# Kernel optimization log

Hardware: AMD Instinct MI355X
Metric: run time of the kernel (lower is better)

Reference implementation:

```python
import jax, jax.numpy as jnp
import numpy as np

ALPHA = 0.2  # LeakyReLU slope in GAT
OUT_SLOPE = 0.01  # default nn.LeakyyReLU slope for self.out
B, E, IN_DIM, HID, HEADS = 4, 2048, 32, 18, 3
DH = HID // HEADS  # per-head out dim = 6


def _leaky(x, slope):
    return jnp.where(x > 0, x, slope * x)


def _gat_head(x, adj, W, a):
    # x: [B,E,in], W: [in,dh], a: [2*dh,1]
    h = jnp.einsum('bei,id->bed', x, W)                      # [B,E,dh]
    d = h.shape[-1]
    # score[b,i,j] = leakyrelu(a . concat(h_i, h_j)) = leakyrelu(h_i.a1 + h_j.a2)
    e1 = jnp.einsum('bed,d->be', h, a[:d, 0])
    e2 = jnp.einsum('bed,d->be', h, a[d:, 0])
    score = _leaky(e1[:, :, None] + e2[:, None, :], ALPHA)   # [B,E,E]
    scores = jnp.where(adj == 1.0, score, 0.0)
    logits = jnp.where(adj > 0.0, scores, -30.0)
    att = jax.nn.softmax(logits, axis=2)                     # softmax over j
    # h_prime[b,j,d] = sum_i att[b,i,j] * h[b,i,d]  (torch sums over dim=1)
    h_prime = jnp.einsum('bij,bid->bjd', att, h)
    return jax.nn.elu(h_prime)  # concat=True -> elu


def _gat_multihead(x, adj, Ws, As):
    # Ws: [H,in,dh], As: [H,2*dh,1]
    outs = jax.vmap(lambda W, a: _gat_head(x, adj, W, a))(Ws, As)  # [H,B,E,dh]
    H, b, e, d = outs.shape
    return jnp.moveaxis(outs, 0, 2).reshape(b, e, H * d)  # concat heads last-dim


def _gcn(x, adj2d, W, b):
    return adj2d @ (x @ W) + b


def setup_inputs() -> dict:
    key = jax.random.key(0)
    ks = jax.random.split(key, 16)
    node_input = jax.random.normal(ks[0], (B, E, IN_DIM), jnp.float32)
    uv_filed = jax.random.normal(ks[1], (B, E, IN_DIM), jnp.float32)
    adj = jax.random.randint(ks[2], (B, E, E), 0, 2).astype(jnp.float32)
    s = 0.1
    Wt1 = jax.random.normal(ks[3], (HEADS, IN_DIM, DH), jnp.float32) * s
    at1 = jax.random.normal(ks[4], (HEADS, 2 * DH, 1), jnp.float32) * s
    Wt2 = jax.random.normal(ks[5], (HEADS, IN_DIM, DH), jnp.float32) * s
    at2 = jax.random.normal(ks[6], (HEADS, 2 * DH, 1), jnp.float32) * s
    Wg1 = jax.random.normal(ks[7], (HID, 16), jnp.float32) * s
    bg1 = jnp.zeros((16,), jnp.float32)
    Wg2 = jax.random.normal(ks[8], (16, 2), jnp.float32) * s
    bg2 = jnp.zeros((2,), jnp.float32)
    Wo1 = jax.random.normal(ks[9], (HID, 16), jnp.float32) * s
    bo1 = jnp.zeros((16,), jnp.float32)
    Wo2 = jax.random.normal(ks[10], (16, 2), jnp.float32) * s
    bo2 = jnp.zeros((2,), jnp.float32)
    return dict(node_input=node_input, uv_filed=uv_filed, adj=adj,
                Wt1=Wt1, at1=at1, Wt2=Wt2, at2=at2,
                Wg1=Wg1, bg1=bg1, Wg2=Wg2, bg2=bg2,
                Wo1=Wo1, bo1=bo1, Wo2=Wo2, bo2=bo2)


def reference(node_input, uv_filed, adj, Wt1, at1, Wt2, at2,
              Wg1, bg1, Wg2, bg2, Wo1, bo1, Wo2, bo2):
    h = _gat_multihead(node_input, adj, Wt1, at1)  # [B,E,18]
    o = _gat_multihead(uv_filed, adj, Wt2, at2)    # [B,E,18]
    a0 = adj[0]
    Y = jax.nn.relu(_gcn(h[0], a0, Wg1, bg1))
    O = jax.nn.relu(_gcn(o[0], a0, Wo1, bo1))
    Y = _gcn(Y, a0, Wg2, bg2)
    O = _gcn(O, a0, Wo2, bo2)
    return (jax.nn.log_softmax(Y, axis=1), _leaky(O, OUT_SLOPE))
```

## Files before the change

kernel.cpp:

```cpp
#include <hip/hip_runtime.h>
#include <hip/hip_bf16.h>


__global__ __launch_bounds__(256) void kA(
    const float* __restrict__ adj0, unsigned int* __restrict__ bm,
    unsigned int* __restrict__ bmT,
    const float* __restrict__ node, const float* __restrict__ uv,
    const float* __restrict__ Wt1, const float* __restrict__ at1,
    const float* __restrict__ Wt2, const float* __restrict__ at2,
    float* __restrict__ hcol, float* __restrict__ pack1, float* __restrict__ pack2) {
  int b = blockIdx.x;
  if (b < 256) {
    int lane = threadIdx.x & 63, w = threadIdx.x >> 6;
    int t = b * 4 + w;
    int ti = t >> 5, tj = t & 31;
    int row = ti * 64 + lane;
    const float4* ar4 = (const float4*)(adj0 + (size_t)row * 2048 + tj * 64);
    unsigned int rowLo = 0, rowHi = 0, myLo = 0, myHi = 0;
#pragma unroll
    for (int it = 0; it < 16; ++it) {
      float4 v = ar4[it];
      unsigned long long m0 = __ballot(v.x == 1.0f);
      unsigned long long m1 = __ballot(v.y == 1.0f);
      unsigned long long m2 = __ballot(v.z == 1.0f);
      unsigned long long m3 = __ballot(v.w == 1.0f);
      int jb = it * 4;
      if (jb + 0 == lane) { myLo = (unsigned int)m0; myHi = (unsigned int)(m0 >> 32); }
      if (jb + 1 == lane) { myLo = (unsigned int)m1; myHi = (unsigned int)(m1 >> 32); }
      if (jb + 2 == lane) { myLo = (unsigned int)m2; myHi = (unsigned int)(m2 >> 32); }
      if (jb + 3 == lane) { myLo = (unsigned int)m3; myHi = (unsigned int)(m3 >> 32); }
      unsigned int rb = (v.x == 1.0f ? 1u : 0u) | (v.y == 1.0f ? 2u : 0u) |
                        (v.z == 1.0f ? 4u : 0u) | (v.w == 1.0f ? 8u : 0u);
      if (it < 8) rowLo |= rb << (it * 4);
      else rowHi |= rb << ((it - 8) * 4);
    }
    *(uint2*)&bm[(size_t)row * 64 + tj * 2] = make_uint2(rowLo, rowHi);
    int j = tj * 64 + lane;
    *(uint2*)&bmT[(size_t)j * 64 + ti * 2] = make_uint2(myLo, myHi);
    return;
  }
  __shared__ float sW[192];
  __shared__ float sA[12];
  int fb = b - 256;
  int g = fb / 24;
  int h = (fb / 8) % 3;
  int e = (fb % 8) * 256 + threadIdx.x;
  const float* W = (g ? Wt2 : Wt1) + h * 192;
  const float* A = (g ? at2 : at1) + h * 12;
  const float* x = (g ? uv : node) + e * 32;
  if (threadIdx.x < 192) sW[threadIdx.x] = W[threadIdx.x];
  if (threadIdx.x < 12) sA[threadIdx.x] = A[threadIdx.x];
  __syncthreads();
  float xv[32];
#pragma unroll
  for (int i = 0; i < 32; ++i) xv[i] = x[i];
  float hv[6];
#pragma unroll
  for (int d = 0; d < 6; ++d) hv[d] = 0.f;
#pragma unroll
  for (int i = 0; i < 32; ++i)
#pragma unroll
    for (int d = 0; d < 6; ++d) hv[d] += xv[i] * sW[i * 6 + d];
  float e1 = 0.f, e2 = 0.f;
#pragma unroll
  for (int d = 0; d < 6; ++d) {
    e1 += hv[d] * sA[d];
    e2 += hv[d] * sA[6 + d];
  }
  int c = g * 3 + h;
#pragma unroll
  for (int d = 0; d < 6; ++d) hcol[(c * 6 + d) * 2048 + e] = hv[d];
  pack1[c * 2048 + e] = e1;
  pack1[(6 + c) * 2048 + e] = __expf(e1);
  pack1[(12 + c) * 2048 + e] = __expf(0.2f * e1);
  pack2[c * 2048 + e] = e2;
  pack2[(6 + c) * 2048 + e] = __expf(e2);
  pack2[(12 + c) * 2048 + e] = __expf(0.2f * e2);
}

__global__ __launch_bounds__(384) void kB(
    const unsigned int* __restrict__ bm, const float* __restrict__ pack1,
    const float* __restrict__ pack2, const float* __restrict__ hcol,
    float* __restrict__ hsS) {
  int tid = threadIdx.x;
  int c = tid >> 6, lane = tid & 63;
  int i0 = blockIdx.x * 8;
  const float4* p2_4 = (const float4*)pack2;
  float e1r[8], p1r[8], q1r[8], sum[8];
#pragma unroll
  for (int r = 0; r < 8; ++r) {
    e1r[r] = pack1[c * 2048 + i0 + r];
    p1r[r] = pack1[(6 + c) * 2048 + i0 + r];
    q1r[r] = pack1[(12 + c) * 2048 + i0 + r];
    sum[r] = 0.f;
  }
  int sh = (lane & 7) * 4;
#pragma unroll
  for (int it = 0; it < 8; ++it) {
    int j4 = it * 64 + lane;
    float4 e2 = p2_4[c * 512 + j4];
    float4 p2 = p2_4[(6 + c) * 512 + j4];
    float4 q2 = p2_4[(12 + c) * 512 + j4];
    int wbase = it * 8 + (lane >> 3);
    float abx, aby, abz, abw;
#pragma unroll
    for (int r = 0; r < 8; ++r) {
      unsigned int wd = bm[(i0 + r) * 64 + wbase] >> sh;
      { float e = e1r[r] + e2.x; bool p = e > 0.f;
        abx = (p ? p1r[r] : q1r[r]) * (p ? p2.x : q2.x); }
      { float e = e1r[r] + e2.y; bool p = e > 0.f;
        aby = (p ? p1r[r] : q1r[r]) * (p ? p2.y : q2.y); }
      { float e = e1r[r] + e2.z; bool p = e > 0.f;
        abz = (p ? p1r[r] : q1r[r]) * (p ? p2.z : q2.z); }
      { float e = e1r[r] + e2.w; bool p = e > 0.f;
        abw = (p ? p1r[r] : q1r[r]) * (p ? p2.w : q2.w); }
      float s = ((wd & 1u) ? abx : 0.f) + ((wd & 2u) ? aby : 0.f) +
                ((wd & 4u) ? abz : 0.f) + ((wd & 8u) ? abw : 0.f);
      sum[r] += s;
    }
  }
#pragma unroll
  for (int r = 0; r < 8; ++r) {
#pragma unroll
    for (int off = 32; off > 0; off >>= 1) sum[r] += __shfl_xor(sum[r], off);
  }
  if (lane < 6) {
    int row = c * 6 + lane;
#pragma unroll
    for (int r = 0; r < 8; ++r) {
      float inv = 1.0f / sum[r];
      hsS[row * 2048 + i0 + r] = hcol[row * 2048 + i0 + r] * inv;
    }
  }
}

__global__ __launch_bounds__(384) void kC(
    const unsigned int* __restrict__ bmT, const float* __restrict__ pack1,
    const float* __restrict__ pack2, const float* __restrict__ hsS,
    const float* __restrict__ Wg1, const float* __restrict__ Wo1,
    float* __restrict__ T) {
  __shared__ float sW[576];
  __shared__ float sHP[4 * 37];
  int tid = threadIdx.x;
  int c = tid >> 6, L = tid & 63;
  int j0 = blockIdx.x * 4;
  if (tid < 288) { sW[tid] = Wg1[tid]; sW[288 + tid] = Wo1[tid]; }
  int wj[4];
#pragma unroll
  for (int jj = 0; jj < 4; ++jj) wj[jj] = (int)bmT[(size_t)(j0 + jj) * 64 + L];
  float e2v[4], p2v[4], q2v[4];
#pragma unroll
  for (int jj = 0; jj < 4; ++jj) {
    e2v[jj] = pack2[c * 2048 + j0 + jj];
    p2v[jj] = pack2[(6 + c) * 2048 + j0 + jj];
    q2v[jj] = pack2[(12 + c) * 2048 + j0 + jj];
  }
  float acc[4][6];
#pragma unroll
  for (int jj = 0; jj < 4; ++jj)
#pragma unroll
    for (int d = 0; d < 6; ++d) acc[jj][d] = 0.f;

  for (int s = 0; s < 32; ++s) {
    int i = s * 64 + L;
    float e1 = pack1[c * 2048 + i];
    float p1 = pack1[(6 + c) * 2048 + i];
    float q1 = pack1[(12 + c) * 2048 + i];
    float h0 = hsS[(c * 6 + 0) * 2048 + i];
    float h1 = hsS[(c * 6 + 1) * 2048 + i];
    float h2 = hsS[(c * 6 + 2) * 2048 + i];
    float h3 = hsS[(c * 6 + 3) * 2048 + i];
    float h4 = hsS[(c * 6 + 4) * 2048 + i];
    float h5 = hsS[(c * 6 + 5) * 2048 + i];
#pragma unroll
    for (int jj = 0; jj < 4; ++jj) {
      int lo = __builtin_amdgcn_readlane(wj[jj], 2 * s);
      int hi = __builtin_amdgcn_readlane(wj[jj], 2 * s + 1);
      unsigned int wsel = (unsigned int)((L & 32) ? hi : lo);
      float e = e1 + e2v[jj];
      bool pos = e > 0.f;
      float ab = (pos ? p1 : q1) * (pos ? p2v[jj] : q2v[jj]);
      float wgt = ((wsel >> (L & 31)) & 1u) ? ab : 0.f;
      acc[jj][0] += wgt * h0; acc[jj][1] += wgt * h1; acc[jj][2] += wgt * h2;
      acc[jj][3] += wgt * h3; acc[jj][4] += wgt * h4; acc[jj][5] += wgt * h5;
    }
  }
#pragma unroll
  for (int jj = 0; jj < 4; ++jj)
#pragma unroll
    for (int d = 0; d < 6; ++d)
#pragma unroll
      for (int off = 32; off > 0; off >>= 1)
        acc[jj][d] += __shfl_xor(acc[jj][d], off);
  if (L == 0) {
#pragma unroll
    for (int jj = 0; jj < 4; ++jj)
#pragma unroll
      for (int d = 0; d < 6; ++d) {
        float x = acc[jj][d];
        sHP[jj * 37 + c * 6 + d] = x > 0.f ? x : __expf(x) - 1.f;
      }
  }
  __syncthreads();
  if (tid < 128) {
    int j = tid >> 5, col = tid & 31;
    int gat = col >> 4, cp = col & 15;
    const float* Wp = sW + gat * 288;
    const float* hp = sHP + j * 37 + gat * 18;
    float a = 0.f;
#pragma unroll
    for (int r = 0; r < 18; ++r) a += hp[r] * Wp[r * 16 + cp];
    T[(size_t)(j0 + j) * 32 + col] = a;
  }
}

__global__ __launch_bounds__(256) void kD(
    const unsigned int* __restrict__ bm, const float* __restrict__ T,
    const float* __restrict__ bg1, const float* __restrict__ bo1,
    const float* __restrict__ Wg2, const float* __restrict__ Wo2,
    float* __restrict__ T2) {
  __shared__ float sC[8 * 32];
  int tid = threadIdx.x;
  int kl = tid & 31, cg = tid >> 5;
  int r0 = blockIdx.x * 8;
  const float4* T4 = (const float4*)T;
  float4 acc[8];
#pragma unroll
  for (int rr = 0; rr < 8; ++rr) acc[rr] = make_float4(0.f, 0.f, 0.f, 0.f);
  for (int ch = 0; ch < 8; ++ch) {
    float4 tv[8];
#pragma unroll
    for (int t = 0; t < 8; ++t)
      tv[t] = T4[(size_t)(ch * 256 + t * 32 + kl) * 8 + cg];
#pragma unroll
    for (int rr = 0; rr < 8; ++rr) {
      const unsigned int* wp = &bm[(size_t)(r0 + rr) * 64 + ch * 8];
      uint4 wA = *(const uint4*)wp;
      uint4 wB = *(const uint4*)(wp + 4);
      float m;
      m = (float)((wA.x >> kl) & 1u);
      acc[rr].x += m * tv[0].x; acc[rr].y += m * tv[0].y;
      acc[rr].z += m * tv[0].z; acc[rr].w += m * tv[0].w;
      m = (float)((wA.y >> kl) & 1u);
      acc[rr].x += m * tv[1].x; acc[rr].y += m * tv[1].y;
      acc[rr].z += m * tv[1].z; acc[rr].w += m * tv[1].w;
      m = (float)((wA.z >> kl) & 1u);
      acc[rr].x += m * tv[2].x; acc[rr].y += m * tv[2].y;
      acc[rr].z += m * tv[2].z; acc[rr].w += m * tv[2].w;
      m = (float)((wA.w >> kl) & 1u);
      acc[rr].x += m * tv[3].x; acc[rr].y += m * tv[3].y;
      acc[rr].z += m * tv[3].z; acc[rr].w += m * tv[3].w;
      m = (float)((wB.x >> kl) & 1u);
      acc[rr].x += m * tv[4].x; acc[rr].y += m * tv[4].y;
      acc[rr].z += m * tv[4].z; acc[rr].w += m * tv[4].w;
      m = (float)((wB.y >> kl) & 1u);
      acc[rr].x += m * tv[5].x; acc[rr].y += m * tv[5].y;
      acc[rr].z += m * tv[5].z; acc[rr].w += m * tv[5].w;
      m = (float)((wB.z >> kl) & 1u);
      acc[rr].x += m * tv[6].x; acc[rr].y += m * tv[6].y;
      acc[rr].z += m * tv[6].z; acc[rr].w += m * tv[6].w;
      m = (float)((wB.w >> kl) & 1u);
      acc[rr].x += m * tv[7].x; acc[rr].y += m * tv[7].y;
      acc[rr].z += m * tv[7].z; acc[rr].w += m * tv[7].w;
    }
  }
#pragma unroll
  for (int rr = 0; rr < 8; ++rr) {
#pragma unroll
    for (int m = 16; m > 0; m >>= 1) {
      acc[rr].x += __shfl_xor(acc[rr].x, m);
      acc[rr].y += __shfl_xor(acc[rr].y, m);
      acc[rr].z += __shfl_xor(acc[rr].z, m);
      acc[rr].w += __shfl_xor(acc[rr].w, m);
    }
  }
  if (kl == 0) {
#pragma unroll
    for (int rr = 0; rr < 8; ++rr)
      *(float4*)&sC[rr * 32 + cg * 4] = acc[rr];
  }
  __syncthreads();
  {
    int r = tid >> 5, col = tid & 31;
    int gat = col >> 4, cc = col & 15;
    float x = sC[r * 32 + col] + (gat ? bo1[cc] : bg1[cc]);
    x = x > 0.f ? x : 0.f;
    float wa = gat ? Wo2[cc * 2 + 0] : Wg2[cc * 2 + 0];
    float wb = gat ? Wo2[cc * 2 + 1] : Wg2[cc * 2 + 1];
    float pa = x * wa, pb = x * wb;
#pragma unroll
    for (int m = 8; m > 0; m >>= 1) {
      pa += __shfl_xor(pa, m);
      pb += __shfl_xor(pb, m);
    }
    if (cc == 0) {
      T2[(size_t)(r0 + r) * 4 + gat * 2 + 0] = pa;
      T2[(size_t)(r0 + r) * 4 + gat * 2 + 1] = pb;
    }
  }
}

__global__ __launch_bounds__(256) void kE(
    const unsigned int* __restrict__ bm, const float* __restrict__ T2,
    const float* __restrict__ bg2, const float* __restrict__ bo2,
    float* __restrict__ out) {
  int tid = threadIdx.x;
  int lane = tid & 63, w = tid >> 6;
  int r = blockIdx.x * 4 + w;
  const float4* T24 = (const float4*)T2;
  float4 acc = make_float4(0.f, 0.f, 0.f, 0.f);
  int sh = lane & 31;
#pragma unroll 8
  for (int it = 0; it < 32; ++it) {
    int k = it * 64 + lane;
    unsigned int wd = bm[r * 64 + it * 2 + (lane >> 5)];
    float m = (float)((wd >> sh) & 1u);
    float4 t = T24[k];
    acc.x += m * t.x;
    acc.y += m * t.y;
    acc.z += m * t.z;
    acc.w += m * t.w;
  }
#pragma unroll
  for (int off = 32; off > 0; off >>= 1) {
    acc.x += __shfl_down(acc.x, off);
    acc.y += __shfl_down(acc.y, off);
    acc.z += __shfl_down(acc.z, off);
    acc.w += __shfl_down(acc.w, off);
  }
  if (lane == 0) {
    float y0 = acc.x + bg2[0], y1 = acc.y + bg2[1];
    float m = fmaxf(y0, y1);
    float ls = m + logf(__expf(y0 - m) + __expf(y1 - m));
    out[r * 2 + 0] = y0 - ls;
    out[r * 2 + 1] = y1 - ls;
    float o0 = acc.z + bo2[0], o1 = acc.w + bo2[1];
    out[4096 + r * 2 + 0] = o0 > 0.f ? o0 : 0.01f * o0;
    out[4096 + r * 2 + 1] = o1 > 0.f ? o1 : 0.01f * o1;
  }
}

extern "C" void kernel_launch(void* const* d_in, const int* in_sizes, int n_in,
                              void* d_out, int out_size, void* d_ws, size_t ws_size,
                              hipStream_t stream) {
  const float* node = (const float*)d_in[0];
  const float* uv = (const float*)d_in[1];
  const float* adj = (const float*)d_in[2];
  const float* Wt1 = (const float*)d_in[3];
  const float* at1 = (const float*)d_in[4];
  const float* Wt2 = (const float*)d_in[5];
  const float* at2 = (const float*)d_in[6];
  const float* Wg1 = (const float*)d_in[7];
  const float* bg1 = (const float*)d_in[8];
  const float* Wg2 = (const float*)d_in[9];
  const float* bg2 = (const float*)d_in[10];
  const float* Wo1 = (const float*)d_in[11];
  const float* bo1 = (const float*)d_in[12];
  const float* Wo2 = (const float*)d_in[13];
  const float* bo2 = (const float*)d_in[14];
  float* ws = (float*)d_ws;
  float* hcol = ws;
  float* pack1 = ws + 73728;
  float* pack2 = ws + 110592;
  float* hsS = ws + 147456;
  float* T = ws + 221184;
  float* T2 = ws + 286720;
  unsigned int* bm = (unsigned int*)(ws + 294912);
  unsigned int* bmT = (unsigned int*)(ws + 425984);
  float* out = (float*)d_out;

  kA<<<304, 256, 0, stream>>>(adj, bm, bmT, node, uv, Wt1, at1, Wt2, at2,
                              hcol, pack1, pack2);
  kB<<<256, 384, 0, stream>>>(bm, pack1, pack2, hcol, hsS);
  kC<<<512, 384, 0, stream>>>(bmT, pack1, pack2, hsS, Wg1, Wo1, T);
  kD<<<256, 256, 0, stream>>>(bm, T, bg1, bo1, Wg2, Wo2, T2);
  kE<<<512, 256, 0, stream>>>(bm, T2, bg2, bo2, out);
}
```

Measured before the change: 171.2 us.

## Fuse four trailing kernels into one persistent kernel with flag-based grid barriers

```diff
diff --git a/kernel.cpp b/kernel.cpp
--- a/kernel.cpp
+++ b/kernel.cpp
@@ -2,14 +2,37 @@
 #include <hip/hip_bf16.h>
 
 
+#define FLAG_BASE 0x15CA0000u
+
+__device__ __forceinline__ void gbar(unsigned* flags, unsigned phase) {
+  __syncthreads();
+  if (threadIdx.x == 0) {
+    __threadfence();
+    __hip_atomic_store(&flags[blockIdx.x], FLAG_BASE + phase,
+                       __ATOMIC_RELAXED, __HIP_MEMORY_SCOPE_AGENT);
+  }
+  for (;;) {
+    int mine = 1;
+    if (threadIdx.x < 256) {
+      unsigned a = __hip_atomic_load(&flags[threadIdx.x],
+                                     __ATOMIC_RELAXED, __HIP_MEMORY_SCOPE_AGENT);
+      mine = ((a >> 16) == (FLAG_BASE >> 16)) & ((a & 0xFFFFu) >= phase);
+    }
+    if (__syncthreads_and(mine)) break;
+    __builtin_amdgcn_s_sleep(2);
+  }
+  __threadfence();
+}
+
 __global__ __launch_bounds__(256) void kA(
     const float* __restrict__ adj0, unsigned int* __restrict__ bm,
-    unsigned int* __restrict__ bmT,
+    unsigned int* __restrict__ bmT, unsigned int* __restrict__ flags,
     const float* __restrict__ node, const float* __restrict__ uv,
     const float* __restrict__ Wt1, const float* __restrict__ at1,
     const float* __restrict__ Wt2, const float* __restrict__ at2,
     float* __restrict__ hcol, float* __restrict__ pack1, float* __restrict__ pack2) {
   int b = blockIdx.x;
+  if (b == 0) flags[threadIdx.x] = FLAG_BASE;
   if (b < 256) {
     int lane = threadIdx.x & 63, w = threadIdx.x >> 6;
     int t = b * 4 + w;
@@ -78,265 +101,269 @@
   pack2[(12 + c) * 2048 + e] = __expf(0.2f * e2);
 }
 
-__global__ __launch_bounds__(384) void kB(
-    const unsigned int* __restrict__ bm, const float* __restrict__ pack1,
-    const float* __restrict__ pack2, const float* __restrict__ hcol,
-    float* __restrict__ hsS) {
+__global__ __launch_bounds__(384, 2) void kBCDE(
+    const unsigned int* __restrict__ bm, const unsigned int* __restrict__ bmT,
+    unsigned int* __restrict__ flags,
+    const float* __restrict__ pack1, const float* __restrict__ pack2,
+    const float* __restrict__ hcol, float* __restrict__ hsS,
+    const float* __restrict__ Wg1, const float* __restrict__ Wo1,
+    float* __restrict__ T,
+    const float* __restrict__ bg1, const float* __restrict__ bo1,
+    const float* __restrict__ Wg2, const float* __restrict__ Wo2,
+    float* __restrict__ T2,
+    const float* __restrict__ bg2, const float* __restrict__ bo2,
+    float* __restrict__ out) {
+  __shared__ float smem[880];
   int tid = threadIdx.x;
   int c = tid >> 6, lane = tid & 63;
-  int i0 = blockIdx.x * 8;
-  const float4* p2_4 = (const float4*)pack2;
-  float e1r[8], p1r[8], q1r[8], sum[8];
-#pragma unroll
-  for (int r = 0; r < 8; ++r) {
-    e1r[r] = pack1[c * 2048 + i0 + r];
-    p1r[r] = pack1[(6 + c) * 2048 + i0 + r];
-    q1r[r] = pack1[(12 + c) * 2048 + i0 + r];
-    sum[r] = 0.f;
-  }
-  int sh = (lane & 7) * 4;
-#pragma unroll
-  for (int it = 0; it < 8; ++it) {
-    int j4 = it * 64 + lane;
-    float4 e2 = p2_4[c * 512 + j4];
-    float4 p2 = p2_4[(6 + c) * 512 + j4];
-    float4 q2 = p2_4[(12 + c) * 512 + j4];
-    int wbase = it * 8 + (lane >> 3);
-    float abx, aby, abz, abw;
+
+  {
+    int i0 = blockIdx.x * 8;
+    const float4* p2_4 = (const float4*)pack2;
+    float e1r[8], p1r[8], q1r[8], sum[8];
 #pragma unroll
     for (int r = 0; r < 8; ++r) {
-      unsigned int wd = bm[(i0 + r) * 64 + wbase] >> sh;
-      { float e = e1r[r] + e2.x; bool p = e > 0.f;
-        abx = (p ? p1r[r] : q1r[r]) * (p ? p2.x : q2.x); }
-      { float e = e1r[r] + e2.y; bool p = e > 0.f;
-        aby = (p ? p1r[r] : q1r[r]) * (p ? p2.y : q2.y); }
-      { float e = e1r[r] + e2.z; bool p = e > 0.f;
-        abz = (p ? p1r[r] : q1r[r]) * (p ? p2.z : q2.z); }
-      { float e = e1r[r] + e2.w; bool p = e > 0.f;
-        abw = (p ? p1r[r] : q1r[r]) * (p ? p2.w : q2.w); }
-      float s = ((wd & 1u) ? abx : 0.f) + ((wd & 2u) ? aby : 0.f) +
-                ((wd & 4u) ? abz : 0.f) + ((wd & 8u) ? abw : 0.f);
-      sum[r] += s;
-    }
-  }
-#pragma unroll
-  for (int r = 0; r < 8; ++r) {
-#pragma unroll
-    for (int off = 32; off > 0; off >>= 1) sum[r] += __shfl_xor(sum[r], off);
-  }
-  if (lane < 6) {
-    int row = c * 6 + lane;
+      e1r[r] = pack1[c * 2048 + i0 + r];
+      p1r[r] = pack1[(6 + c) * 2048 + i0 + r];
+      q1r[r] = pack1[(12 + c) * 2048 + i0 + r];
+      sum[r] = 0.f;
+    }
+    int sh = (lane & 7) * 4;
+#pragma unroll
+    for (int it = 0; it < 8; ++it) {
+      int j4 = it * 64 + lane;
+      float4 e2 = p2_4[c * 512 + j4];
+      float4 p2 = p2_4[(6 + c) * 512 + j4];
+      float4 q2 = p2_4[(12 + c) * 512 + j4];
+      int wbase = it * 8 + (lane >> 3);
+      float abx, aby, abz, abw;
+#pragma unroll
+      for (int r = 0; r < 8; ++r) {
+        unsigned int wd = bm[(i0 + r) * 64 + wbase] >> sh;
+        { float e = e1r[r] + e2.x; bool p = e > 0.f;
+          abx = (p ? p1r[r] : q1r[r]) * (p ? p2.x : q2.x); }
+        { float e = e1r[r] + e2.y; bool p = e > 0.f;
+          aby = (p ? p1r[r] : q1r[r]) * (p ? p2.y : q2.y); }
+        { float e = e1r[r] + e2.z; bool p = e > 0.f;
+          abz = (p ? p1r[r] : q1r[r]) * (p ? p2.z : q2.z); }
+        { float e = e1r[r] + e2.w; bool p = e > 0.f;
+          abw = (p ? p1r[r] : q1r[r]) * (p ? p2.w : q2.w); }
+        float s = ((wd & 1u) ? abx : 0.f) + ((wd & 2u) ? aby : 0.f) +
+                  ((wd & 4u) ? abz : 0.f) + ((wd & 8u) ? abw : 0.f);
+        sum[r] += s;
+      }
+    }
 #pragma unroll
     for (int r = 0; r < 8; ++r) {
-      float inv = 1.0f / sum[r];
-      hsS[row * 2048 + i0 + r] = hcol[row * 2048 + i0 + r] * inv;
-    }
-  }
-}
-
-__global__ __launch_bounds__(384) void kC(
-    const unsigned int* __restrict__ bmT, const float* __restrict__ pack1,
-    const float* __restrict__ pack2, const float* __restrict__ hsS,
-    const float* __restrict__ Wg1, const float* __restrict__ Wo1,
-    float* __restrict__ T) {
-  __shared__ float sW[576];
-  __shared__ float sHP[4 * 37];
-  int tid = threadIdx.x;
-  int c = tid >> 6, L = tid & 63;
-  int j0 = blockIdx.x * 4;
-  if (tid < 288) { sW[tid] = Wg1[tid]; sW[288 + tid] = Wo1[tid]; }
-  int wj[4];
-#pragma unroll
-  for (int jj = 0; jj < 4; ++jj) wj[jj] = (int)bmT[(size_t)(j0 + jj) * 64 + L];
-  float e2v[4], p2v[4], q2v[4];
-#pragma unroll
-  for (int jj = 0; jj < 4; ++jj) {
-    e2v[jj] = pack2[c * 2048 + j0 + jj];
-    p2v[jj] = pack2[(6 + c) * 2048 + j0 + jj];
-    q2v[jj] = pack2[(12 + c) * 2048 + j0 + jj];
-  }
-  float acc[4][6];
-#pragma unroll
-  for (int jj = 0; jj < 4; ++jj)
-#pragma unroll
-    for (int d = 0; d < 6; ++d) acc[jj][d] = 0.f;
-
-  for (int s = 0; s < 32; ++s) {
-    int i = s * 64 + L;
-    float e1 = pack1[c * 2048 + i];
-    float p1 = pack1[(6 + c) * 2048 + i];
-    float q1 = pack1[(12 + c) * 2048 + i];
-    float h0 = hsS[(c * 6 + 0) * 2048 + i];
-    float h1 = hsS[(c * 6 + 1) * 2048 + i];
-    float h2 = hsS[(c * 6 + 2) * 2048 + i];
-    float h3 = hsS[(c * 6 + 3) * 2048 + i];
-    float h4 = hsS[(c * 6 + 4) * 2048 + i];
-    float h5 = hsS[(c * 6 + 5) * 2048 + i];
-#pragma unroll
-    for (int jj = 0; jj < 4; ++jj) {
-      int lo = __builtin_amdgcn_readlane(wj[jj], 2 * s);
-      int hi = __builtin_amdgcn_readlane(wj[jj], 2 * s + 1);
-      unsigned int wsel = (unsigned int)((L & 32) ? hi : lo);
-      float e = e1 + e2v[jj];
-      bool pos = e > 0.f;
-      float ab = (pos ? p1 : q1) * (pos ? p2v[jj] : q2v[jj]);
-      float wgt = ((wsel >> (L & 31)) & 1u) ? ab : 0.f;
-      acc[jj][0] += wgt * h0; acc[jj][1] += wgt * h1; acc[jj][2] += wgt * h2;
-      acc[jj][3] += wgt * h3; acc[jj][4] += wgt * h4; acc[jj][5] += wgt * h5;
-    }
-  }
-#pragma unroll
-  for (int jj = 0; jj < 4; ++jj)
-#pragma unroll
-    for (int d = 0; d < 6; ++d)
-#pragma unroll
-      for (int off = 32; off > 0; off >>= 1)
-        acc[jj][d] += __shfl_xor(acc[jj][d], off);
-  if (L == 0) {
-#pragma unroll
-    for (int jj = 0; jj < 4; ++jj)
-#pragma unroll
-      for (int d = 0; d < 6; ++d) {
-        float x = acc[jj][d];
-        sHP[jj * 37 + c * 6 + d] = x > 0.f ? x : __expf(x) - 1.f;
-      }
-  }
-  __syncthreads();
-  if (tid < 128) {
-    int j = tid >> 5, col = tid & 31;
-    int gat = col >> 4, cp = col & 15;
-    const float* Wp = sW + gat * 288;
-    const float* hp = sHP + j * 37 + gat * 18;
-    float a = 0.f;
-#pragma unroll
-    for (int r = 0; r < 18; ++r) a += hp[r] * Wp[r * 16 + cp];
-    T[(size_t)(j0 + j) * 32 + col] = a;
-  }
-}
-
-__global__ __launch_bounds__(256) void kD(
-    const unsigned int* __restrict__ bm, const float* __restrict__ T,
-    const float* __restrict__ bg1, const float* __restrict__ bo1,
-    const float* __restrict__ Wg2, const float* __restrict__ Wo2,
-    float* __restrict__ T2) {
-  __shared__ float sC[8 * 32];
-  int tid = threadIdx.x;
-  int kl = tid & 31, cg = tid >> 5;
-  int r0 = blockIdx.x * 8;
-  const float4* T4 = (const float4*)T;
-  float4 acc[8];
-#pragma unroll
-  for (int rr = 0; rr < 8; ++rr) acc[rr] = make_float4(0.f, 0.f, 0.f, 0.f);
-  for (int ch = 0; ch < 8; ++ch) {
-    float4 tv[8];
-#pragma unroll
-    for (int t = 0; t < 8; ++t)
-      tv[t] = T4[(size_t)(ch * 256 + t * 32 + kl) * 8 + cg];
-#pragma unroll
-    for (int rr = 0; rr < 8; ++rr) {
-      const unsigned int* wp = &bm[(size_t)(r0 + rr) * 64 + ch * 8];
-      uint4 wA = *(const uint4*)wp;
-      uint4 wB = *(const uint4*)(wp + 4);
-      float m;
-      m = (float)((wA.x >> kl) & 1u);
-      acc[rr].x += m * tv[0].x; acc[rr].y += m * tv[0].y;
-      acc[rr].z += m * tv[0].z; acc[rr].w += m * tv[0].w;
-      m = (float)((wA.y >> kl) & 1u);
-      acc[rr].x += m * tv[1].x; acc[rr].y += m * tv[1].y;
-      acc[rr].z += m * tv[1].z; acc[rr].w += m * tv[1].w;
-      m = (float)((wA.z >> kl) & 1u);
-      acc[rr].x += m * tv[2].x; acc[rr].y += m * tv[2].y;
-      acc[rr].z += m * tv[2].z; acc[rr].w += m * tv[2].w;
-      m = (float)((wA.w >> kl) & 1u);
-      acc[rr].x += m * tv[3].x; acc[rr].y += m * tv[3].y;
-      acc[rr].z += m * tv[3].z; acc[rr].w += m * tv[3].w;
-      m = (float)((wB.x >> kl) & 1u);
-      acc[rr].x += m * tv[4].x; acc[rr].y += m * tv[4].y;
-      acc[rr].z += m * tv[4].z; acc[rr].w += m * tv[4].w;
-      m = (float)((wB.y >> kl) & 1u);
-      acc[rr].x += m * tv[5].x; acc[rr].y += m * tv[5].y;
-      acc[rr].z += m * tv[5].z; acc[rr].w += m * tv[5].w;
-      m = (float)((wB.z >> kl) & 1u);
-      acc[rr].x += m * tv[6].x; acc[rr].y += m * tv[6].y;
-      acc[rr].z += m * tv[6].z; acc[rr].w += m * tv[6].w;
-      m = (float)((wB.w >> kl) & 1u);
-      acc[rr].x += m * tv[7].x; acc[rr].y += m * tv[7].y;
-      acc[rr].z += m * tv[7].z; acc[rr].w += m * tv[7].w;
-    }
-  }
-#pragma unroll
-  for (int rr = 0; rr < 8; ++rr) {
-#pragma unroll
-    for (int m = 16; m > 0; m >>= 1) {
-      acc[rr].x += __shfl_xor(acc[rr].x, m);
-      acc[rr].y += __shfl_xor(acc[rr].y, m);
-      acc[rr].z += __shfl_xor(acc[rr].z, m);
-      acc[rr].w += __shfl_xor(acc[rr].w, m);
-    }
-  }
-  if (kl == 0) {
-#pragma unroll
-    for (int rr = 0; rr < 8; ++rr)
-      *(float4*)&sC[rr * 32 + cg * 4] = acc[rr];
-  }
-  __syncthreads();
+#pragma unroll
+      for (int off = 32; off > 0; off >>= 1) sum[r] += __shfl_xor(sum[r], off);
+    }
+    if (lane < 6) {
+      int row = c * 6 + lane;
+#pragma unroll
+      for (int r = 0; r < 8; ++r) {
+        float inv = 1.0f / sum[r];
+        hsS[row * 2048 + i0 + r] = hcol[row * 2048 + i0 + r] * inv;
+      }
+    }
+  }
+  gbar(flags, 1);
+
   {
-    int r = tid >> 5, col = tid & 31;
-    int gat = col >> 4, cc = col & 15;
-    float x = sC[r * 32 + col] + (gat ? bo1[cc] : bg1[cc]);
-    x = x > 0.f ? x : 0.f;
-    float wa = gat ? Wo2[cc * 2 + 0] : Wg2[cc * 2 + 0];
-    float wb = gat ? Wo2[cc * 2 + 1] : Wg2[cc * 2 + 1];
-    float pa = x * wa, pb = x * wb;
-#pragma unroll
-    for (int m = 8; m > 0; m >>= 1) {
-      pa += __shfl_xor(pa, m);
-      pb += __shfl_xor(pb, m);
-    }
-    if (cc == 0) {
-      T2[(size_t)(r0 + r) * 4 + gat * 2 + 0] = pa;
-      T2[(size_t)(r0 + r) * 4 + gat * 2 + 1] = pb;
-    }
-  }
-}
-
-__global__ __launch_bounds__(256) void kE(
-    const unsigned int* __restrict__ bm, const float* __restrict__ T2,
-    const float* __restrict__ bg2, const float* __restrict__ bo2,
-    float* __restrict__ out) {
-  int tid = threadIdx.x;
-  int lane = tid & 63, w = tid >> 6;
-  int r = blockIdx.x * 4 + w;
-  const float4* T24 = (const float4*)T2;
-  float4 acc = make_float4(0.f, 0.f, 0.f, 0.f);
-  int sh = lane & 31;
+    float* sW = smem;
+    float* sHP = smem + 576;
+    int j0 = blockIdx.x * 8;
+    if (tid < 288) { sW[tid] = Wg1[tid]; sW[288 + tid] = Wo1[tid]; }
+    int wj[8];
+#pragma unroll
+    for (int jj = 0; jj < 8; ++jj) wj[jj] = (int)bmT[(size_t)(j0 + jj) * 64 + lane];
+    float e2v[8], p2v[8], q2v[8];
+#pragma unroll
+    for (int jj = 0; jj < 8; ++jj) {
+      e2v[jj] = pack2[c * 2048 + j0 + jj];
+      p2v[jj] = pack2[(6 + c) * 2048 + j0 + jj];
+      q2v[jj] = pack2[(12 + c) * 2048 + j0 + jj];
+    }
+    float acc[8][6];
+#pragma unroll
+    for (int jj = 0; jj < 8; ++jj)
+#pragma unroll
+      for (int d = 0; d < 6; ++d) acc[jj][d] = 0.f;
+
+    for (int s = 0; s < 32; ++s) {
+      int i = s * 64 + lane;
+      float e1 = pack1[c * 2048 + i];
+      float p1 = pack1[(6 + c) * 2048 + i];
+      float q1 = pack1[(12 + c) * 2048 + i];
+      float h0 = hsS[(c * 6 + 0) * 2048 + i];
+      float h1 = hsS[(c * 6 + 1) * 2048 + i];
+      float h2 = hsS[(c * 6 + 2) * 2048 + i];
+      float h3 = hsS[(c * 6 + 3) * 2048 + i];
+      float h4 = hsS[(c * 6 + 4) * 2048 + i];
+      float h5 = hsS[(c * 6 + 5) * 2048 + i];
+#pragma unroll
+      for (int jj = 0; jj < 8; ++jj) {
+        int lo = __builtin_amdgcn_readlane(wj[jj], 2 * s);
+        int hi = __builtin_amdgcn_readlane(wj[jj], 2 * s + 1);
+        unsigned int wsel = (unsigned int)((lane & 32) ? hi : lo);
+        float e = e1 + e2v[jj];
+        bool pos = e > 0.f;
+        float ab = (pos ? p1 : q1) * (pos ? p2v[jj] : q2v[jj]);
+        float wgt = ((wsel >> (lane & 31)) & 1u) ? ab : 0.f;
+        acc[jj][0] += wgt * h0; acc[jj][1] += wgt * h1; acc[jj][2] += wgt * h2;
+        acc[jj][3] += wgt * h3; acc[jj][4] += wgt * h4; acc[jj][5] += wgt * h5;
+      }
+    }
+#pragma unroll
+    for (int jj = 0; jj < 8; ++jj)
+#pragma unroll
+      for (int d = 0; d < 6; ++d)
+#pragma unroll
+        for (int off = 32; off > 0; off >>= 1)
+          acc[jj][d] += __shfl_xor(acc[jj][d], off);
+    if (lane == 0) {
+#pragma unroll
+      for (int jj = 0; jj < 8; ++jj)
+#pragma unroll
+        for (int d = 0; d < 6; ++d) {
+          float x = acc[jj][d];
+          sHP[jj * 37 + c * 6 + d] = x > 0.f ? x : __expf(x) - 1.f;
+        }
+    }
+    __syncthreads();
+    if (tid < 256) {
+      int j = tid >> 5, col = tid & 31;
+      int gat = col >> 4, cp = col & 15;
+      const float* Wp = sW + gat * 288;
+      const float* hp = sHP + j * 37 + gat * 18;
+      float a = 0.f;
+#pragma unroll
+      for (int r = 0; r < 18; ++r) a += hp[r] * Wp[r * 16 + cp];
+      T[(size_t)(j0 + j) * 32 + col] = a;
+    }
+  }
+  gbar(flags, 2);
+
+  {
+    float* sC = smem;
+    int r0 = blockIdx.x * 8;
+    if (tid < 256) {
+      int kl = tid & 31, cg = tid >> 5;
+      const float4* T4 = (const float4*)T;
+      float4 acc[8];
+#pragma unroll
+      for (int rr = 0; rr < 8; ++rr) acc[rr] = make_float4(0.f, 0.f, 0.f, 0.f);
+      for (int ch = 0; ch < 8; ++ch) {
+        float4 tv[8];
+#pragma unroll
+        for (int t = 0; t < 8; ++t)
+          tv[t] = T4[(size_t)(ch * 256 + t * 32 + kl) * 8 + cg];
+#pragma unroll
+        for (int rr = 0; rr < 8; ++rr) {
+          const unsigned int* wp = &bm[(size_t)(r0 + rr) * 64 + ch * 8];
+          uint4 wA = *(const uint4*)wp;
+          uint4 wB = *(const uint4*)(wp + 4);
+          float m;
+          m = (float)((wA.x >> kl) & 1u);
+          acc[rr].x += m * tv[0].x; acc[rr].y += m * tv[0].y;
+          acc[rr].z += m * tv[0].z; acc[rr].w += m * tv[0].w;
+          m = (float)((wA.y >> kl) & 1u);
+          acc[rr].x += m * tv[1].x; acc[rr].y += m * tv[1].y;
+          acc[rr].z += m * tv[1].z; acc[rr].w += m * tv[1].w;
+          m = (float)((wA.z >> kl) & 1u);
+          acc[rr].x += m * tv[2].x; acc[rr].y += m * tv[2].y;
+          acc[rr].z += m * tv[2].z; acc[rr].w += m * tv[2].w;
+          m = (float)((wA.w >> kl) & 1u);
+          acc[rr].x += m * tv[3].x; acc[rr].y += m * tv[3].y;
+          acc[rr].z += m * tv[3].z; acc[rr].w += m * tv[3].w;
+          m = (float)((wB.x >> kl) & 1u);
+          acc[rr].x += m * tv[4].x; acc[rr].y += m * tv[4].y;
+          acc[rr].z += m * tv[4].z; acc[rr].w += m * tv[4].w;
+          m = (float)((wB.y >> kl) & 1u);
+          acc[rr].x += m * tv[5].x; acc[rr].y += m * tv[5].y;
+          acc[rr].z += m * tv[5].z; acc[rr].w += m * tv[5].w;
+          m = (float)((wB.z >> kl) & 1u);
+          acc[rr].x += m * tv[6].x; acc[rr].y += m * tv[6].y;
+          acc[rr].z += m * tv[6].z; acc[rr].w += m * tv[6].w;
+          m = (float)((wB.w >> kl) & 1u);
+          acc[rr].x += m * tv[7].x; acc[rr].y += m * tv[7].y;
+          acc[rr].z += m * tv[7].z; acc[rr].w += m * tv[7].w;
+        }
+      }
+#pragma unroll
+      for (int rr = 0; rr < 8; ++rr) {
+#pragma unroll
+        for (int m = 16; m > 0; m >>= 1) {
+          acc[rr].x += __shfl_xor(acc[rr].x, m);
+          acc[rr].y += __shfl_xor(acc[rr].y, m);
+          acc[rr].z += __shfl_xor(acc[rr].z, m);
+          acc[rr].w += __shfl_xor(acc[rr].w, m);
+        }
+      }
+      if (kl == 0) {
+#pragma unroll
+        for (int rr = 0; rr < 8; ++rr)
+          *(float4*)&sC[rr * 32 + cg * 4] = acc[rr];
+      }
+    }
+    __syncthreads();
+    if (tid < 256) {
+      int r = tid >> 5, col = tid & 31;
+      int gat = col >> 4, cc = col & 15;
+      float x = sC[r * 32 + col] + (gat ? bo1[cc] : bg1[cc]);
+      x = x > 0.f ? x : 0.f;
+      float wa = gat ? Wo2[cc * 2 + 0] : Wg2[cc * 2 + 0];
+      float wb = gat ? Wo2[cc * 2 + 1] : Wg2[cc * 2 + 1];
+      float pa = x * wa, pb = x * wb;
+#pragma unroll
+      for (int m = 8; m > 0; m >>= 1) {
+        pa += __shfl_xor(pa, m);
+        pb += __shfl_xor(pb, m);
+      }
+      if (cc == 0) {
+        T2[(size_t)(r0 + r) * 4 + gat * 2 + 0] = pa;
+        T2[(size_t)(r0 + r) * 4 + gat * 2 + 1] = pb;
+      }
+    }
+  }
+  gbar(flags, 3);
+
+  {
+    int wv = tid >> 6;
+    for (int rr = wv; rr < 8; rr += 6) {
+      int r = blockIdx.x * 8 + rr;
+      const float4* T24 = (const float4*)T2;
+      float4 acc = make_float4(0.f, 0.f, 0.f, 0.f);
+      int sh = lane & 31;
 #pragma unroll 8
-  for (int it = 0; it < 32; ++it) {
-    int k = it * 64 + lane;
-    unsigned int wd = bm[r * 64 + it * 2 + (lane >> 5)];
-    float m = (float)((wd >> sh) & 1u);
-    float4 t = T24[k];
-    acc.x += m * t.x;
-    acc.y += m * t.y;
-    acc.z += m * t.z;
-    acc.w += m * t.w;
-  }
-#pragma unroll
-  for (int off = 32; off > 0; off >>= 1) {
-    acc.x += __shfl_down(acc.x, off);
-    acc.y += __shfl_down(acc.y, off);
-    acc.z += __shfl_down(acc.z, off);
-    acc.w += __shfl_down(acc.w, off);
-  }
-  if (lane == 0) {
-    float y0 = acc.x + bg2[0], y1 = acc.y + bg2[1];
-    float m = fmaxf(y0, y1);
-    float ls = m + logf(__expf(y0 - m) + __expf(y1 - m));
-    out[r * 2 + 0] = y0 - ls;
-    out[r * 2 + 1] = y1 - ls;
-    float o0 = acc.z + bo2[0], o1 = acc.w + bo2[1];
-    out[4096 + r * 2 + 0] = o0 > 0.f ? o0 : 0.01f * o0;
-    out[4096 + r * 2 + 1] = o1 > 0.f ? o1 : 0.01f * o1;
+      for (int it = 0; it < 32; ++it) {
+        int k = it * 64 + lane;
+        unsigned int wd = bm[r * 64 + it * 2 + (lane >> 5)];
+        float m = (float)((wd >> sh) & 1u);
+        float4 t = T24[k];
+        acc.x += m * t.x;
+        acc.y += m * t.y;
+        acc.z += m * t.z;
+        acc.w += m * t.w;
+      }
+#pragma unroll
+      for (int off = 32; off > 0; off >>= 1) {
+        acc.x += __shfl_down(acc.x, off);
+        acc.y += __shfl_down(acc.y, off);
+        acc.z += __shfl_down(acc.z, off);
+        acc.w += __shfl_down(acc.w, off);
+      }
+      if (lane == 0) {
+        float y0 = acc.x + bg2[0], y1 = acc.y + bg2[1];
+        float m = fmaxf(y0, y1);
+        float ls = m + logf(__expf(y0 - m) + __expf(y1 - m));
+        out[r * 2 + 0] = y0 - ls;
+        out[r * 2 + 1] = y1 - ls;
+        float o0 = acc.z + bo2[0], o1 = acc.w + bo2[1];
+        out[4096 + r * 2 + 0] = o0 > 0.f ? o0 : 0.01f * o0;
+        out[4096 + r * 2 + 1] = o1 > 0.f ? o1 : 0.01f * o1;
+      }
+    }
   }
 }
 
@@ -367,12 +394,12 @@
   float* T2 = ws + 286720;
   unsigned int* bm = (unsigned int*)(ws + 294912);
   unsigned int* bmT = (unsigned int*)(ws + 425984);
+  unsigned int* flags = (unsigned int*)(ws + 557056);
   float* out = (float*)d_out;
 
-  kA<<<304, 256, 0, stream>>>(adj, bm, bmT, node, uv, Wt1, at1, Wt2, at2,
+  kA<<<304, 256, 0, stream>>>(adj, bm, bmT, flags, node, uv, Wt1, at1, Wt2, at2,
                               hcol, pack1, pack2);
-  kB<<<256, 384, 0, stream>>>(bm, pack1, pack2, hcol, hsS);
-  kC<<<512, 384, 0, stream>>>(bmT, pack1, pack2, hsS, Wg1, Wo1, T);
-  kD<<<256, 256, 0, stream>>>(bm, T, bg1, bo1, Wg2, Wo2, T2);
-  kE<<<512, 256, 0, stream>>>(bm, T2, bg2, bo2, out);
+  kBCDE<<<256, 384, 0, stream>>>(bm, bmT, flags, pack1, pack2, hcol, hsS,
+                                 Wg1, Wo1, T, bg1, bo1, Wg2, Wo2, T2,
+                                 bg2, bo2, out);
 }
```

Measured after the change: 257.6 us. 50.5% more time.

## Pack per-node records into AoS, prefetch in kC, halve rows per block

Applied to the files above, without the earlier changes.

```diff
diff --git a/kernel.cpp b/kernel.cpp
--- a/kernel.cpp
+++ b/kernel.cpp
@@ -81,14 +81,14 @@
 __global__ __launch_bounds__(384) void kB(
     const unsigned int* __restrict__ bm, const float* __restrict__ pack1,
     const float* __restrict__ pack2, const float* __restrict__ hcol,
-    float* __restrict__ hsS) {
+    float* __restrict__ crec) {
   int tid = threadIdx.x;
   int c = tid >> 6, lane = tid & 63;
-  int i0 = blockIdx.x * 8;
+  int i0 = blockIdx.x * 4;
   const float4* p2_4 = (const float4*)pack2;
-  float e1r[8], p1r[8], q1r[8], sum[8];
-#pragma unroll
-  for (int r = 0; r < 8; ++r) {
+  float e1r[4], p1r[4], q1r[4], sum[4];
+#pragma unroll
+  for (int r = 0; r < 4; ++r) {
     e1r[r] = pack1[c * 2048 + i0 + r];
     p1r[r] = pack1[(6 + c) * 2048 + i0 + r];
     q1r[r] = pack1[(12 + c) * 2048 + i0 + r];
@@ -104,7 +104,7 @@
     int wbase = it * 8 + (lane >> 3);
     float abx, aby, abz, abw;
 #pragma unroll
-    for (int r = 0; r < 8; ++r) {
+    for (int r = 0; r < 4; ++r) {
       unsigned int wd = bm[(i0 + r) * 64 + wbase] >> sh;
       { float e = e1r[r] + e2.x; bool p = e > 0.f;
         abx = (p ? p1r[r] : q1r[r]) * (p ? p2.x : q2.x); }
@@ -120,23 +120,29 @@
     }
   }
 #pragma unroll
-  for (int r = 0; r < 8; ++r) {
+  for (int r = 0; r < 4; ++r) {
 #pragma unroll
     for (int off = 32; off > 0; off >>= 1) sum[r] += __shfl_xor(sum[r], off);
   }
-  if (lane < 6) {
-    int row = c * 6 + lane;
-#pragma unroll
-    for (int r = 0; r < 8; ++r) {
-      float inv = 1.0f / sum[r];
-      hsS[row * 2048 + i0 + r] = hcol[row * 2048 + i0 + r] * inv;
-    }
+  if (lane < 4) {
+    int r = lane;
+    int i = i0 + r;
+    float inv = 1.0f / sum[r];
+    float h0 = hcol[(c * 6 + 0) * 2048 + i] * inv;
+    float h1 = hcol[(c * 6 + 1) * 2048 + i] * inv;
+    float h2 = hcol[(c * 6 + 2) * 2048 + i] * inv;
+    float h3 = hcol[(c * 6 + 3) * 2048 + i] * inv;
+    float h4 = hcol[(c * 6 + 4) * 2048 + i] * inv;
+    float h5 = hcol[(c * 6 + 5) * 2048 + i] * inv;
+    float4* c4 = (float4*)crec;
+    c4[(size_t)(c * 2048 + i) * 2 + 0] = make_float4(e1r[r], p1r[r], h0, h1);
+    c4[(size_t)(c * 2048 + i) * 2 + 1] = make_float4(h2, h3, h4, h5);
   }
 }
 
 __global__ __launch_bounds__(384) void kC(
-    const unsigned int* __restrict__ bmT, const float* __restrict__ pack1,
-    const float* __restrict__ pack2, const float* __restrict__ hsS,
+    const unsigned int* __restrict__ bmT, const float* __restrict__ crec,
+    const float* __restrict__ pack2,
     const float* __restrict__ Wg1, const float* __restrict__ Wo1,
     float* __restrict__ T) {
   __shared__ float sW[576];
@@ -161,17 +167,18 @@
 #pragma unroll
     for (int d = 0; d < 6; ++d) acc[jj][d] = 0.f;
 
+  const float4* R4 = (const float4*)crec;
+  int base = c * 2048 + L;
+  float4 a0 = R4[(size_t)base * 2];
+  float4 a1 = R4[(size_t)base * 2 + 1];
   for (int s = 0; s < 32; ++s) {
-    int i = s * 64 + L;
-    float e1 = pack1[c * 2048 + i];
-    float p1 = pack1[(6 + c) * 2048 + i];
-    float q1 = pack1[(12 + c) * 2048 + i];
-    float h0 = hsS[(c * 6 + 0) * 2048 + i];
-    float h1 = hsS[(c * 6 + 1) * 2048 + i];
-    float h2 = hsS[(c * 6 + 2) * 2048 + i];
-    float h3 = hsS[(c * 6 + 3) * 2048 + i];
-    float h4 = hsS[(c * 6 + 4) * 2048 + i];
-    float h5 = hsS[(c * 6 + 5) * 2048 + i];
+    int nb = base + (((s + 1) & 31) << 6);
+    float4 b0 = R4[(size_t)nb * 2];
+    float4 b1 = R4[(size_t)nb * 2 + 1];
+    float e1 = a0.x, p1 = a0.y;
+    float q1 = __expf(0.2f * e1);
+    float h0 = a0.z, h1 = a0.w;
+    float h2 = a1.x, h3 = a1.y, h4 = a1.z, h5 = a1.w;
 #pragma unroll
     for (int jj = 0; jj < 4; ++jj) {
       int lo = __builtin_amdgcn_readlane(wj[jj], 2 * s);
@@ -184,6 +191,7 @@
       acc[jj][0] += wgt * h0; acc[jj][1] += wgt * h1; acc[jj][2] += wgt * h2;
       acc[jj][3] += wgt * h3; acc[jj][4] += wgt * h4; acc[jj][5] += wgt * h5;
     }
+    a0 = b0; a1 = b1;
   }
 #pragma unroll
   for (int jj = 0; jj < 4; ++jj)
@@ -219,21 +227,21 @@
     const float* __restrict__ bg1, const float* __restrict__ bo1,
     const float* __restrict__ Wg2, const float* __restrict__ Wo2,
     float* __restrict__ T2) {
-  __shared__ float sC[8 * 32];
+  __shared__ float sC[4 * 32];
   int tid = threadIdx.x;
   int kl = tid & 31, cg = tid >> 5;
-  int r0 = blockIdx.x * 8;
+  int r0 = blockIdx.x * 4;
   const float4* T4 = (const float4*)T;
-  float4 acc[8];
-#pragma unroll
-  for (int rr = 0; rr < 8; ++rr) acc[rr] = make_float4(0.f, 0.f, 0.f, 0.f);
+  float4 acc[4];
+#pragma unroll
+  for (int rr = 0; rr < 4; ++rr) acc[rr] = make_float4(0.f, 0.f, 0.f, 0.f);
   for (int ch = 0; ch < 8; ++ch) {
     float4 tv[8];
 #pragma unroll
     for (int t = 0; t < 8; ++t)
       tv[t] = T4[(size_t)(ch * 256 + t * 32 + kl) * 8 + cg];
 #pragma unroll
-    for (int rr = 0; rr < 8; ++rr) {
+    for (int rr = 0; rr < 4; ++rr) {
       const unsigned int* wp = &bm[(size_t)(r0 + rr) * 64 + ch * 8];
       uint4 wA = *(const uint4*)wp;
       uint4 wB = *(const uint4*)(wp + 4);
@@ -265,7 +273,7 @@
     }
   }
 #pragma unroll
-  for (int rr = 0; rr < 8; ++rr) {
+  for (int rr = 0; rr < 4; ++rr) {
 #pragma unroll
     for (int m = 16; m > 0; m >>= 1) {
       acc[rr].x += __shfl_xor(acc[rr].x, m);
@@ -276,11 +284,11 @@
   }
   if (kl == 0) {
 #pragma unroll
-    for (int rr = 0; rr < 8; ++rr)
+    for (int rr = 0; rr < 4; ++rr)
       *(float4*)&sC[rr * 32 + cg * 4] = acc[rr];
   }
   __syncthreads();
-  {
+  if (tid < 128) {
     int r = tid >> 5, col = tid & 31;
     int gat = col >> 4, cc = col & 15;
     float x = sC[r * 32 + col] + (gat ? bo1[cc] : bg1[cc]);
@@ -362,17 +370,17 @@
   float* hcol = ws;
   float* pack1 = ws + 73728;
   float* pack2 = ws + 110592;
-  float* hsS = ws + 147456;
-  float* T = ws + 221184;
-  float* T2 = ws + 286720;
-  unsigned int* bm = (unsigned int*)(ws + 294912);
-  unsigned int* bmT = (unsigned int*)(ws + 425984);
+  float* crec = ws + 147456;
+  float* T = ws + 245760;
+  float* T2 = ws + 311296;
+  unsigned int* bm = (unsigned int*)(ws + 319488);
+  unsigned int* bmT = (unsigned int*)(ws + 450560);
   float* out = (float*)d_out;
 
   kA<<<304, 256, 0, stream>>>(adj, bm, bmT, node, uv, Wt1, at1, Wt2, at2,
                               hcol, pack1, pack2);
-  kB<<<256, 384, 0, stream>>>(bm, pack1, pack2, hcol, hsS);
-  kC<<<512, 384, 0, stream>>>(bmT, pack1, pack2, hsS, Wg1, Wo1, T);
-  kD<<<256, 256, 0, stream>>>(bm, T, bg1, bo1, Wg2, Wo2, T2);
+  kB<<<512, 384, 0, stream>>>(bm, pack1, pack2, hcol, crec);
+  kC<<<512, 384, 0, stream>>>(bmT, crec, pack2, Wg1, Wo1, T);
+  kD<<<512, 256, 0, stream>>>(bm, T, bg1, bo1, Wg2, Wo2, T2);
   kE<<<512, 256, 0, stream>>>(bm, T2, bg2, bo2, out);
 }
```

Measured after the change: 177.9 us. 3.9% more time.

## Fuse kB and kC into one kernel with flag-based inter-block sync

Applied to the files above, without the earlier changes.

```diff
diff --git a/kernel.cpp b/kernel.cpp
--- a/kernel.cpp
+++ b/kernel.cpp
@@ -2,14 +2,18 @@
 #include <hip/hip_bf16.h>
 
 
+#define FLAG_INIT 0x15CA0000u
+#define FLAG_SET  0x15CA0001u
+
 __global__ __launch_bounds__(256) void kA(
     const float* __restrict__ adj0, unsigned int* __restrict__ bm,
-    unsigned int* __restrict__ bmT,
+    unsigned int* __restrict__ bmT, unsigned int* __restrict__ flags,
     const float* __restrict__ node, const float* __restrict__ uv,
     const float* __restrict__ Wt1, const float* __restrict__ at1,
     const float* __restrict__ Wt2, const float* __restrict__ at2,
     float* __restrict__ hcol, float* __restrict__ pack1, float* __restrict__ pack2) {
   int b = blockIdx.x;
+  if (b == 0) flags[threadIdx.x] = FLAG_INIT;
   if (b < 256) {
     int lane = threadIdx.x & 63, w = threadIdx.x >> 6;
     int t = b * 4 + w;
@@ -78,72 +82,77 @@
   pack2[(12 + c) * 2048 + e] = __expf(0.2f * e2);
 }
 
-__global__ __launch_bounds__(384) void kB(
-    const unsigned int* __restrict__ bm, const float* __restrict__ pack1,
-    const float* __restrict__ pack2, const float* __restrict__ hcol,
-    float* __restrict__ hsS) {
-  int tid = threadIdx.x;
-  int c = tid >> 6, lane = tid & 63;
-  int i0 = blockIdx.x * 8;
-  const float4* p2_4 = (const float4*)pack2;
-  float e1r[8], p1r[8], q1r[8], sum[8];
-#pragma unroll
-  for (int r = 0; r < 8; ++r) {
-    e1r[r] = pack1[c * 2048 + i0 + r];
-    p1r[r] = pack1[(6 + c) * 2048 + i0 + r];
-    q1r[r] = pack1[(12 + c) * 2048 + i0 + r];
-    sum[r] = 0.f;
-  }
-  int sh = (lane & 7) * 4;
-#pragma unroll
-  for (int it = 0; it < 8; ++it) {
-    int j4 = it * 64 + lane;
-    float4 e2 = p2_4[c * 512 + j4];
-    float4 p2 = p2_4[(6 + c) * 512 + j4];
-    float4 q2 = p2_4[(12 + c) * 512 + j4];
-    int wbase = it * 8 + (lane >> 3);
-    float abx, aby, abz, abw;
-#pragma unroll
-    for (int r = 0; r < 8; ++r) {
-      unsigned int wd = bm[(i0 + r) * 64 + wbase] >> sh;
-      { float e = e1r[r] + e2.x; bool p = e > 0.f;
-        abx = (p ? p1r[r] : q1r[r]) * (p ? p2.x : q2.x); }
-      { float e = e1r[r] + e2.y; bool p = e > 0.f;
-        aby = (p ? p1r[r] : q1r[r]) * (p ? p2.y : q2.y); }
-      { float e = e1r[r] + e2.z; bool p = e > 0.f;
-        abz = (p ? p1r[r] : q1r[r]) * (p ? p2.z : q2.z); }
-      { float e = e1r[r] + e2.w; bool p = e > 0.f;
-        abw = (p ? p1r[r] : q1r[r]) * (p ? p2.w : q2.w); }
-      float s = ((wd & 1u) ? abx : 0.f) + ((wd & 2u) ? aby : 0.f) +
-                ((wd & 4u) ? abz : 0.f) + ((wd & 8u) ? abw : 0.f);
-      sum[r] += s;
-    }
-  }
-#pragma unroll
-  for (int r = 0; r < 8; ++r) {
-#pragma unroll
-    for (int off = 32; off > 0; off >>= 1) sum[r] += __shfl_xor(sum[r], off);
-  }
-  if (lane < 6) {
-    int row = c * 6 + lane;
-#pragma unroll
-    for (int r = 0; r < 8; ++r) {
-      float inv = 1.0f / sum[r];
-      hsS[row * 2048 + i0 + r] = hcol[row * 2048 + i0 + r] * inv;
-    }
-  }
-}
-
-__global__ __launch_bounds__(384) void kC(
-    const unsigned int* __restrict__ bmT, const float* __restrict__ pack1,
-    const float* __restrict__ pack2, const float* __restrict__ hsS,
+__global__ __launch_bounds__(384, 4) void kBC(
+    const unsigned int* __restrict__ bm, const unsigned int* __restrict__ bmT,
+    unsigned int* __restrict__ flags,
+    const float* __restrict__ pack1, const float* __restrict__ pack2,
+    const float* __restrict__ hcol, float* __restrict__ hsS,
     const float* __restrict__ Wg1, const float* __restrict__ Wo1,
     float* __restrict__ T) {
   __shared__ float sW[576];
   __shared__ float sHP[4 * 37];
   int tid = threadIdx.x;
   int c = tid >> 6, L = tid & 63;
-  int j0 = blockIdx.x * 4;
+  int b = blockIdx.x;
+
+  if (b < 256) {
+    int i0 = b * 8;
+    const float4* p2_4 = (const float4*)pack2;
+    float e1r[8], p1r[8], q1r[8], sum[8];
+#pragma unroll
+    for (int r = 0; r < 8; ++r) {
+      e1r[r] = pack1[c * 2048 + i0 + r];
+      p1r[r] = pack1[(6 + c) * 2048 + i0 + r];
+      q1r[r] = pack1[(12 + c) * 2048 + i0 + r];
+      sum[r] = 0.f;
+    }
+    int sh = (L & 7) * 4;
+#pragma unroll
+    for (int it = 0; it < 8; ++it) {
+      int j4 = it * 64 + L;
+      float4 e2 = p2_4[c * 512 + j4];
+      float4 p2 = p2_4[(6 + c) * 512 + j4];
+      float4 q2 = p2_4[(12 + c) * 512 + j4];
+      int wbase = it * 8 + (L >> 3);
+      float abx, aby, abz, abw;
+#pragma unroll
+      for (int r = 0; r < 8; ++r) {
+        unsigned int wd = bm[(i0 + r) * 64 + wbase] >> sh;
+        { float e = e1r[r] + e2.x; bool p = e > 0.f;
+          abx = (p ? p1r[r] : q1r[r]) * (p ? p2.x : q2.x); }
+        { float e = e1r[r] + e2.y; bool p = e > 0.f;
+          aby = (p ? p1r[r] : q1r[r]) * (p ? p2.y : q2.y); }
+        { float e = e1r[r] + e2.z; bool p = e > 0.f;
+          abz = (p ? p1r[r] : q1r[r]) * (p ? p2.z : q2.z); }
+        { float e = e1r[r] + e2.w; bool p = e > 0.f;
+          abw = (p ? p1r[r] : q1r[r]) * (p ? p2.w : q2.w); }
+        float s = ((wd & 1u) ? abx : 0.f) + ((wd & 2u) ? aby : 0.f) +
+                  ((wd & 4u) ? abz : 0.f) + ((wd & 8u) ? abw : 0.f);
+        sum[r] += s;
+      }
+    }
+#pragma unroll
+    for (int r = 0; r < 8; ++r) {
+#pragma unroll
+      for (int off = 32; off > 0; off >>= 1) sum[r] += __shfl_xor(sum[r], off);
+    }
+    if (L < 6) {
+      int row = c * 6 + L;
+#pragma unroll
+      for (int r = 0; r < 8; ++r) {
+        float inv = 1.0f / sum[r];
+        hsS[row * 2048 + i0 + r] = hcol[row * 2048 + i0 + r] * inv;
+      }
+    }
+    __syncthreads();
+    if (tid == 0) {
+      __threadfence();
+      __hip_atomic_store(&flags[b], FLAG_SET, __ATOMIC_RELAXED,
+                         __HIP_MEMORY_SCOPE_AGENT);
+    }
+  }
+
+  int j0 = b * 4;
   if (tid < 288) { sW[tid] = Wg1[tid]; sW[288 + tid] = Wo1[tid]; }
   int wj[4];
 #pragma unroll
@@ -155,6 +164,25 @@
     p2v[jj] = pack2[(6 + c) * 2048 + j0 + jj];
     q2v[jj] = pack2[(12 + c) * 2048 + j0 + jj];
   }
+  for (;;) {
+    int good;
+    {
+      unsigned f0 = __hip_atomic_load(&flags[L], __ATOMIC_RELAXED,
+                                      __HIP_MEMORY_SCOPE_AGENT);
+      unsigned f1 = __hip_atomic_load(&flags[64 + L], __ATOMIC_RELAXED,
+                                      __HIP_MEMORY_SCOPE_AGENT);
+      unsigned f2 = __hip_atomic_load(&flags[128 + L], __ATOMIC_RELAXED,
+                                      __HIP_MEMORY_SCOPE_AGENT);
+      unsigned f3 = __hip_atomic_load(&flags[192 + L], __ATOMIC_RELAXED,
+                                      __HIP_MEMORY_SCOPE_AGENT);
+      good = (f0 == FLAG_SET) & (f1 == FLAG_SET) &
+             (f2 == FLAG_SET) & (f3 == FLAG_SET);
+    }
+    if (__all(good)) break;
+    __builtin_amdgcn_s_sleep(2);
+  }
+  __threadfence();
+
   float acc[4][6];
 #pragma unroll
   for (int jj = 0; jj < 4; ++jj)
@@ -367,12 +395,13 @@
   float* T2 = ws + 286720;
   unsigned int* bm = (unsigned int*)(ws + 294912);
   unsigned int* bmT = (unsigned int*)(ws + 425984);
+  unsigned int* flags = (unsigned int*)(ws + 557056);
   float* out = (float*)d_out;
 
-  kA<<<304, 256, 0, stream>>>(adj, bm, bmT, node, uv, Wt1, at1, Wt2, at2,
+  kA<<<304, 256, 0, stream>>>(adj, bm, bmT, flags, node, uv, Wt1, at1, Wt2, at2,
                               hcol, pack1, pack2);
-  kB<<<256, 384, 0, stream>>>(bm, pack1, pack2, hcol, hsS);
-  kC<<<512, 384, 0, stream>>>(bmT, pack1, pack2, hsS, Wg1, Wo1, T);
+  kBC<<<512, 384, 0, stream>>>(bm, bmT, flags, pack1, pack2, hcol, hsS,
+                               Wg1, Wo1, T);
   kD<<<256, 256, 0, stream>>>(bm, T, bg1, bo1, Wg2, Wo2, T2);
   kE<<<512, 256, 0, stream>>>(bm, T2, bg2, bo2, out);
 }
```

Result: slower. 273.1 us (+59.6%).
